# Kernel optimization log

Hardware: AMD Instinct MI355X
Metric: run time of the kernel (lower is better)

The kernel has to match this reference:

```python
import jax, jax.numpy as jnp
import numpy as np

N = 65536      # tokens
H = 8          # num_heads
D = 64         # head_dim
G = 64         # num_slices
HID = H * D    # 512
EPS = 1e-5
SCALE = float(1.0 / np.sqrt(D))


def _lin(k, out_dim, in_dim):
    return (jax.random.normal(k, (out_dim, in_dim), jnp.float32) / np.sqrt(in_dim)).astype(jnp.float32)


def setup_inputs() -> dict:
    key = jax.random.key(0)
    ks = jax.random.split(key, 12)
    return {
        "x": jax.random.normal(ks[0], (N, HID), jnp.float32),
        "W_x": _lin(ks[1], HID, HID), "b_x": jnp.zeros((HID,), jnp.float32),
        "W_slice": _lin(ks[2], G, D), "b_slice": jnp.zeros((G,), jnp.float32),
        "W_t1": _lin(ks[3], G, D), "b_t1": jnp.zeros((G,), jnp.float32),
        "W_t2": _lin(ks[4], 1, G), "b_t2": jnp.zeros((1,), jnp.float32),
        "t_bias": jnp.ones((H, 1, 1), jnp.float32) * 0.5,
        "Wq": _lin(ks[5], D, D), "Wk": _lin(ks[6], D, D),
        "Wv": _lin(ks[7], D, D), "Wo": _lin(ks[8], D, D),
        "W_out": _lin(ks[9], HID, HID), "b_out": jnp.zeros((HID,), jnp.float32),
    }


def reference(x, W_x, b_x, W_slice, b_slice, W_t1, b_t1, W_t2, b_t2,
              t_bias, Wq, Wk, Wv, Wo, W_out, b_out):
    # project and split heads: [N,HID] -> [H,N,D]
    xp = x @ W_x.T + b_x
    x_mid = jnp.transpose(xp.reshape(-1, H, D), (1, 0, 2))

    # per-token temperature MLP: Linear(D,G) -> gelu -> Linear(G,1) -> gelu, + bias
    t = jax.nn.gelu(jax.nn.gelu(x_mid @ W_t1.T + b_t1) @ W_t2.T + b_t2) + t_bias
    t = jnp.clip(t, 0.01)  # [H,N,1]

    # slice logits + gumbel softmax routing weights [H,N,G]
    logits = x_mid @ W_slice.T + b_slice
    u = jax.random.uniform(jax.random.key(1), logits.shape, jnp.float32)
    gnoise = -jnp.log(-jnp.log(u + 1e-8) + 1e-8)
    w = jax.nn.softmax((logits + gnoise) / t, axis=-1)

    # weighted pooling into G slice tokens per head: [H,G,D]
    norm = w.sum(axis=1)  # [H,G]
    tokens = jnp.einsum('hnd,hng->hgd', x_mid, w) / (norm[..., None] + EPS)

    # tiny single-head self-attention over G slice tokens (shared weights, vmapped over H)
    q = tokens @ Wq.T
    k = tokens @ Wk.T
    v = tokens @ Wv.T
    attn = jax.nn.softmax(jnp.einsum('hgd,hGd->hgG', q * SCALE, k), axis=-1)
    o = jnp.einsum('hgG,hGd->hgd', attn, v) @ Wo.T  # [H,G,D]

    # weighted scatter-back to tokens, merge heads, output projection
    out = jnp.einsum('hgd,hng->hnd', o, w)
    out = jnp.transpose(out, (1, 0, 2)).reshape(-1, HID)
    return out @ W_out.T + b_out
```

## Files before the change

### kernel.cpp

```cpp
#include <hip/hip_runtime.h>
#include <stdint.h>

typedef unsigned short u16;
typedef __bf16 bf16x8 __attribute__((ext_vector_type(8)));
typedef float f32x4 __attribute__((ext_vector_type(4)));


__device__ __forceinline__ u16 f2bf(float f) {
  uint32_t u = __float_as_uint(f);
  uint32_t r = u + 0x7fffu + ((u >> 16) & 1u);
  return (u16)(r >> 16);
}
__device__ __forceinline__ float bf2f(u16 h) {
  return __uint_as_float(((uint32_t)h) << 16);
}

union BF8 { bf16x8 v; u16 u[8]; uint4 q4; };

__device__ __forceinline__ float gelu_fast(float x) {
  const float c = 0.79788456080286535588f;
  float z = c * fmaf(0.044715f, x * x * x, x);
  return x / (1.0f + __expf(-2.0f * z));
}

__device__ __forceinline__ uint32_t rotl32(uint32_t v, int s) {
  return (v << s) | (v >> (32 - s));
}

__device__ __forceinline__ uint32_t threefry_bits(uint32_t idx) {
  const uint32_t k0 = 0u, k1 = 1u;
  const uint32_t k2 = 0x1BD11BDAu ^ k0 ^ k1;
  uint32_t x0 = 0u + k0;
  uint32_t x1 = idx + k1;
#define TF_R(r) { x0 += x1; x1 = rotl32(x1, r); x1 ^= x0; }
  TF_R(13) TF_R(15) TF_R(26) TF_R(6)
  x0 += k1; x1 += k2 + 1u;
  TF_R(17) TF_R(29) TF_R(16) TF_R(24)
  x0 += k2; x1 += k0 + 2u;
  TF_R(13) TF_R(15) TF_R(26) TF_R(6)
  x0 += k0; x1 += k1 + 3u;
  TF_R(17) TF_R(29) TF_R(16) TF_R(24)
  x0 += k1; x1 += k2 + 4u;
  TF_R(13) TF_R(15) TF_R(26) TF_R(6)
  x0 += k2; x1 += k0 + 5u;
#undef TF_R
  return x0 ^ x1;
}

__device__ __forceinline__ void gload_lds16(const void* g, void* l) {
  __builtin_amdgcn_global_load_lds(
      (const __attribute__((address_space(1))) void*)g,
      (__attribute__((address_space(3))) void*)l, 16, 0, 0);
}

__global__ __launch_bounds__(256) void conv_split(
    const float* __restrict__ in, u16* __restrict__ hi, u16* __restrict__ lo,
    int nq)
{
  for (int i = blockIdx.x * 256 + threadIdx.x; i < nq; i += gridDim.x * 256) {
    float4 v = ((const float4*)in)[i];
    ushort4 h, l;
    h.x = f2bf(v.x); l.x = f2bf(v.x - bf2f(h.x));
    h.y = f2bf(v.y); l.y = f2bf(v.y - bf2f(h.y));
    h.z = f2bf(v.z); l.z = f2bf(v.z - bf2f(h.z));
    h.w = f2bf(v.w); l.w = f2bf(v.w - bf2f(h.w));
    ((ushort4*)hi)[i] = h;
    ((ushort4*)lo)[i] = l;
  }
}

__global__ __launch_bounds__(256) void gemm_split(
    const u16* __restrict__ Ah, const u16* __restrict__ Al,
    const u16* __restrict__ Bh, const u16* __restrict__ Bl,
    const float* __restrict__ bias, float* __restrict__ C)
{
  __shared__ u16 lds[4][4096];
  const int tid = threadIdx.x;
  const int lane = tid & 63;
  const int w = tid >> 6;
  const int vid = (blockIdx.x & 7) * 256 + (blockIdx.x >> 3);
  const int bn = vid & 3;
  const int bm = vid >> 2;
  const int wr = w >> 1, wc = w & 1;

  f32x4 acc[4][4];
#pragma unroll
  for (int m = 0; m < 4; ++m)
#pragma unroll
    for (int n = 0; n < 4; ++n) acc[m][n] = (f32x4){0.f, 0.f, 0.f, 0.f};

  const int srow = lane >> 2;
  const int scol = (lane & 3) * 8;

  for (int kt = 0; kt < 16; ++kt) {
    const int k0 = kt * 32;
    __syncthreads();
#pragma unroll
    for (int i = 0; i < 8; ++i) {
      const int mat = i & 3;
      const int rb = w * 2 + (i >> 2);
      const int row = rb * 16 + srow;
      const u16* base = (mat == 0) ? Ah : (mat == 1) ? Al
                       : (mat == 2) ? Bh : Bl;
      const int tbase = (mat < 2) ? bm * 128 : bn * 128;
      const u16* src = base + (size_t)(tbase + row) * 512 + k0 + scol;
      gload_lds16(src, &lds[mat][rb * 512]);
    }
    __syncthreads();

    bf16x8 ah[4], al[4], bh_[4], bl_[4];
    const int co = (lane >> 4) * 8;
    const int rr = lane & 15;
#pragma unroll
    for (int f = 0; f < 4; ++f) {
      const int ra  = (wr * 64 + f * 16 + rr) * 32 + co;
      const int rb2 = (wc * 64 + f * 16 + rr) * 32 + co;
      ah[f]  = *(const bf16x8*)&lds[0][ra];
      al[f]  = *(const bf16x8*)&lds[1][ra];
      bh_[f] = *(const bf16x8*)&lds[2][rb2];
      bl_[f] = *(const bf16x8*)&lds[3][rb2];
    }
#pragma unroll
    for (int m = 0; m < 4; ++m)
#pragma unroll
      for (int n = 0; n < 4; ++n) {
        acc[m][n] = __builtin_amdgcn_mfma_f32_16x16x32_bf16(ah[m], bh_[n], acc[m][n], 0, 0, 0);
        acc[m][n] = __builtin_amdgcn_mfma_f32_16x16x32_bf16(ah[m], bl_[n], acc[m][n], 0, 0, 0);
        acc[m][n] = __builtin_amdgcn_mfma_f32_16x16x32_bf16(al[m], bh_[n], acc[m][n], 0, 0, 0);
      }
  }

  const int cn0 = lane & 15;
  const int rm0 = (lane >> 4) * 4;
#pragma unroll
  for (int n = 0; n < 4; ++n) {
    const int ng = bn * 128 + wc * 64 + n * 16 + cn0;
    const float bv = bias[ng];
#pragma unroll
    for (int m = 0; m < 4; ++m) {
      const int mg = bm * 128 + wr * 64 + m * 16 + rm0;
#pragma unroll
      for (int r = 0; r < 4; ++r)
        C[(size_t)(mg + r) * 512 + ng] = acc[m][n][r] + bv;
    }
  }
}

__global__ __launch_bounds__(256) void gemm_packA(
    const uint32_t* __restrict__ A, const u16* __restrict__ Bh,
    const u16* __restrict__ Bl, const float* __restrict__ bias,
    float* __restrict__ C)
{
  __shared__ uint32_t ldsA[128 * 32];
  __shared__ u16 ldsBh[128 * 32], ldsBl[128 * 32];
  const int tid = threadIdx.x;
  const int lane = tid & 63;
  const int w = tid >> 6;
  const int vid = (blockIdx.x & 7) * 256 + (blockIdx.x >> 3);
  const int bn = vid & 3;
  const int bm = vid >> 2;
  const int wr = w >> 1, wcq = w & 1;

  f32x4 acc[4][4];
#pragma unroll
  for (int m = 0; m < 4; ++m)
#pragma unroll
    for (int n = 0; n < 4; ++n) acc[m][n] = (f32x4){0.f, 0.f, 0.f, 0.f};

  for (int kt = 0; kt < 16; ++kt) {
    const int k0 = kt * 32;
    __syncthreads();
#pragma unroll
    for (int i = 0; i < 4; ++i) {
      const int rb8 = i * 4 + w;
      const int row = rb8 * 8 + (lane >> 3);
      const uint32_t* src =
          A + (size_t)(bm * 128 + row) * 512 + k0 + (lane & 7) * 4;
      gload_lds16(src, &ldsA[rb8 * 8 * 32]);
    }
#pragma unroll
    for (int i = 0; i < 2; ++i) {
      const int rb16 = i * 4 + w;
      const int row = rb16 * 16 + (lane >> 2);
      const int sc = (lane & 3) * 8;
      gload_lds16(Bh + (size_t)(bn * 128 + row) * 512 + k0 + sc,
                  &ldsBh[rb16 * 16 * 32]);
      gload_lds16(Bl + (size_t)(bn * 128 + row) * 512 + k0 + sc,
                  &ldsBl[rb16 * 16 * 32]);
    }
    __syncthreads();

    bf16x8 ah[4], al[4], bh_[4], bl_[4];
    const int co = (lane >> 4) * 8;
    const int rr = lane & 15;
#pragma unroll
    for (int f = 0; f < 4; ++f) {
      const int ra = (wr * 64 + f * 16 + rr) * 32 + co;
      const uint4 p0 = *(const uint4*)&ldsA[ra];
      const uint4 p1 = *(const uint4*)&ldsA[ra + 4];
      BF8 hv, lv;
      uint32_t* hd = (uint32_t*)&hv.q4;
      uint32_t* ld = (uint32_t*)&lv.q4;
      hd[0] = __builtin_amdgcn_perm(p0.y, p0.x, 0x05040100u);
      hd[1] = __builtin_amdgcn_perm(p0.w, p0.z, 0x05040100u);
      hd[2] = __builtin_amdgcn_perm(p1.y, p1.x, 0x05040100u);
      hd[3] = __builtin_amdgcn_perm(p1.w, p1.z, 0x05040100u);
      ld[0] = __builtin_amdgcn_perm(p0.y, p0.x, 0x07060302u);
      ld[1] = __builtin_amdgcn_perm(p0.w, p0.z, 0x07060302u);
      ld[2] = __builtin_amdgcn_perm(p1.y, p1.x, 0x07060302u);
      ld[3] = __builtin_amdgcn_perm(p1.w, p1.z, 0x07060302u);
      ah[f] = hv.v; al[f] = lv.v;
      const int rb2 = (wcq * 64 + f * 16 + rr) * 32 + co;
      bh_[f] = *(const bf16x8*)&ldsBh[rb2];
      bl_[f] = *(const bf16x8*)&ldsBl[rb2];
    }
#pragma unroll
    for (int m = 0; m < 4; ++m)
#pragma unroll
      for (int n = 0; n < 4; ++n) {
        acc[m][n] = __builtin_amdgcn_mfma_f32_16x16x32_bf16(ah[m], bh_[n], acc[m][n], 0, 0, 0);
        acc[m][n] = __builtin_amdgcn_mfma_f32_16x16x32_bf16(ah[m], bl_[n], acc[m][n], 0, 0, 0);
        acc[m][n] = __builtin_amdgcn_mfma_f32_16x16x32_bf16(al[m], bh_[n], acc[m][n], 0, 0, 0);
      }
  }

  const int cn0 = lane & 15;
  const int rm0 = (lane >> 4) * 4;
#pragma unroll
  for (int n = 0; n < 4; ++n) {
    const int ng = bn * 128 + wcq * 64 + n * 16 + cn0;
    const float bv = bias[ng];
#pragma unroll
    for (int m = 0; m < 4; ++m) {
      const int mg = bm * 128 + wr * 64 + m * 16 + rm0;
#pragma unroll
      for (int r = 0; r < 4; ++r)
        C[(size_t)(mg + r) * 512 + ng] = acc[m][n][r] + bv;
    }
  }
}

__global__ __launch_bounds__(256, 4) void k2_route(
    const float* __restrict__ xp, const float* __restrict__ Wsl,
    const float* __restrict__ bsl, const float* __restrict__ Wt1,
    const float* __restrict__ bt1, const float* __restrict__ Wt2,
    const float* __restrict__ bt2, const float* __restrict__ tbias,
    uint32_t* __restrict__ wcp)
{
  __shared__ u16 Wf[2][8][2][64][8];
  __shared__ uint32_t wbuf[4][16][68];

  const int tid = threadIdx.x;
  const int l = tid & 63, wid = tid >> 6;
  const int l15 = l & 15, q = l >> 4;
  const int h = blockIdx.x >> 8;
  const int chunk = blockIdx.x & 255;

#pragma unroll
  for (int it = 0; it < 8; ++it) {
    const int slot = tid + it * 256;
    const int p = slot >> 10;
    const int rest = slot & 1023;
    const int nn = rest >> 7;
    const int kk = (rest >> 6) & 1;
    const int sl = rest & 63;
    const int row = nn * 16 + (sl & 15);
    const int kb = kk * 32 + (sl >> 4) * 8;
    const float* src = (row < 64) ? (Wsl + row * 64 + kb)
                                  : (Wt1 + (row - 64) * 64 + kb);
#pragma unroll
    for (int e = 0; e < 8; ++e) {
      const float v = src[e];
      const u16 hb = f2bf(v);
      Wf[p][nn][kk][sl][e] = (p == 0) ? hb : f2bf(v - bf2f(hb));
    }
  }
  __syncthreads();

  float bslv[4], bt1v[4], wt2v[4];
#pragma unroll
  for (int j = 0; j < 4; ++j) {
    bslv[j] = bsl[j * 16 + l15];
    bt1v[j] = bt1[j * 16 + l15];
    wt2v[j] = Wt2[j * 16 + l15];
  }
  const float bt2v = bt2[0], tbv = tbias[h];

#pragma unroll 1
  for (int tm = 0; tm < 4; ++tm) {
    const int n0t = chunk * 256 + (tm >> 1) * 128 + wid * 32 + (tm & 1) * 16;

    bf16x8 ah[2], al[2];
#pragma unroll
    for (int kk = 0; kk < 2; ++kk) {
      const float* sp = xp + (size_t)(n0t + l15) * 512 + h * 64
                        + kk * 32 + q * 8;
      float4 v0 = *(const float4*)sp;
      float4 v1 = *(const float4*)(sp + 4);
      float vv[8] = {v0.x, v0.y, v0.z, v0.w, v1.x, v1.y, v1.z, v1.w};
      BF8 hv, lv;
#pragma unroll
      for (int e = 0; e < 8; ++e) {
        const u16 hb = f2bf(vv[e]);
        hv.u[e] = hb;
        lv.u[e] = f2bf(vv[e] - bf2f(hb));
      }
      ah[kk] = hv.v; al[kk] = lv.v;
    }

    f32x4 acc[8];
#pragma unroll
    for (int n = 0; n < 8; ++n) acc[n] = (f32x4){0.f, 0.f, 0.f, 0.f};
#pragma unroll
    for (int kk = 0; kk < 2; ++kk)
#pragma unroll
      for (int nn = 0; nn < 8; ++nn) {
        BF8 whf, wlf;
        whf.q4 = *(const uint4*)&Wf[0][nn][kk][l][0];
        wlf.q4 = *(const uint4*)&Wf[1][nn][kk][l][0];
        acc[nn] = __builtin_amdgcn_mfma_f32_16x16x32_bf16(ah[kk], whf.v, acc[nn], 0, 0, 0);
        acc[nn] = __builtin_amdgcn_mfma_f32_16x16x32_bf16(ah[kk], wlf.v, acc[nn], 0, 0, 0);
        acc[nn] = __builtin_amdgcn_mfma_f32_16x16x32_bf16(al[kk], whf.v, acc[nn], 0, 0, 0);
      }

    float itv[4];
#pragma unroll
    for (int r = 0; r < 4; ++r) {
      float part = 0.f;
#pragma unroll
      for (int j = 0; j < 4; ++j)
        part += gelu_fast(acc[4 + j][r] + bt1v[j]) * wt2v[j];
      part += __shfl_xor(part, 1);
      part += __shfl_xor(part, 2);
      part += __shfl_xor(part, 4);
      part += __shfl_xor(part, 8);
      const float tval = gelu_fast(part + bt2v) + tbv;
      itv[r] = 1.0f / fmaxf(tval, 0.01f);
    }

    const uint32_t pbase = ((uint32_t)((h << 16) | (n0t + q * 4))) << 6;
#pragma unroll
    for (int j = 0; j < 4; ++j) {
      const uint32_t cc = j * 16 + l15;
#pragma unroll
      for (int r = 0; r < 4; ++r) {
        const uint32_t bits = threefry_bits(pbase + ((uint32_t)r << 6) + cc);
        const float u = __uint_as_float((bits >> 9) | 0x3f800000u) - 1.0f;
        const float gin = -__logf(u + 1e-8f);
        const float gn = -__logf(gin + 1e-8f);
        acc[j][r] = (acc[j][r] + bslv[j] + gn) * itv[r];
      }
    }

#pragma unroll
    for (int r = 0; r < 4; ++r) {
      float mx = fmaxf(fmaxf(acc[0][r], acc[1][r]),
                       fmaxf(acc[2][r], acc[3][r]));
      mx = fmaxf(mx, __shfl_xor(mx, 1));
      mx = fmaxf(mx, __shfl_xor(mx, 2));
      mx = fmaxf(mx, __shfl_xor(mx, 4));
      mx = fmaxf(mx, __shfl_xor(mx, 8));
      float se = 0.f;
#pragma unroll
      for (int j = 0; j < 4; ++j) {
        const float e = __expf(acc[j][r] - mx);
        acc[j][r] = e;
        se += e;
      }
      se += __shfl_xor(se, 1);
      se += __shfl_xor(se, 2);
      se += __shfl_xor(se, 4);
      se += __shfl_xor(se, 8);
      const float inv = 1.0f / se;
#pragma unroll
      for (int j = 0; j < 4; ++j) acc[j][r] *= inv;
    }

#pragma unroll
    for (int j = 0; j < 4; ++j)
#pragma unroll
      for (int r = 0; r < 4; ++r) {
        const float wv = acc[j][r];
        const u16 hb = f2bf(wv);
        const u16 lb = f2bf(wv - bf2f(hb));
        wbuf[wid][q * 4 + r][j * 16 + l15] = (uint32_t)hb | ((uint32_t)lb << 16);
      }
    __syncthreads();

#pragma unroll
    for (int it = 0; it < 4; ++it) {
      const int t = l >> 2;
      const int qq = (l & 3) + it * 4;
      const uint4 v = *(const uint4*)&wbuf[wid][t][qq * 4];
      *(uint4*)(wcp + (size_t)(n0t + t) * 512 + h * 64 + qq * 4) = v;
    }
    __syncthreads();
  }
}

__global__ __launch_bounds__(256) void k3_pool(
    const float* __restrict__ xp, const uint32_t* __restrict__ wcp,
    float* __restrict__ tok_num, float* __restrict__ nrm)
{
  __shared__ float red[64][65];
  __shared__ float redn[64];
  const int h = blockIdx.x >> 7;
  const int chunk = blockIdx.x & 127;
  const int lane = threadIdx.x & 63;
  const int wid = threadIdx.x >> 6;
  const int i0 = (lane & 7) * 8;
  const int j0 = (lane >> 3) * 8;
  const int jq = lane >> 3;

  float acc[8][8];
#pragma unroll
  for (int j = 0; j < 8; ++j)
#pragma unroll
    for (int i = 0; i < 8; ++i) acc[j][i] = 0.f;
  float csum[8];
#pragma unroll
  for (int j = 0; j < 8; ++j) csum[j] = 0.f;

  const int n0 = chunk * 512 + wid * 128;
  const size_t base0 = (size_t)n0 * 512 + h * 64;

  float4 nx0 = *(const float4*)(xp + base0 + i0);
  float4 nx1 = *(const float4*)(xp + base0 + i0 + 4);
  uint4 nq0 = *(const uint4*)(wcp + base0 + j0);
  uint4 nq1 = *(const uint4*)(wcp + base0 + j0 + 4);

#pragma unroll 2
  for (int t = 0; t < 128; ++t) {
    const float4 x0 = nx0, x1 = nx1;
    const uint4 q0 = nq0, q1 = nq1;
    if (t < 127) {
      const size_t nb = base0 + (size_t)(t + 1) * 512;
      nx0 = *(const float4*)(xp + nb + i0);
      nx1 = *(const float4*)(xp + nb + i0 + 4);
      nq0 = *(const uint4*)(wcp + nb + j0);
      nq1 = *(const uint4*)(wcp + nb + j0 + 4);
    }
    const float x8[8] = {x0.x, x0.y, x0.z, x0.w, x1.x, x1.y, x1.z, x1.w};
    const float w8[8] = {
        __uint_as_float(q0.x << 16) + __uint_as_float(q0.x & 0xffff0000u),
        __uint_as_float(q0.y << 16) + __uint_as_float(q0.y & 0xffff0000u),
        __uint_as_float(q0.z << 16) + __uint_as_float(q0.z & 0xffff0000u),
        __uint_as_float(q0.w << 16) + __uint_as_float(q0.w & 0xffff0000u),
        __uint_as_float(q1.x << 16) + __uint_as_float(q1.x & 0xffff0000u),
        __uint_as_float(q1.y << 16) + __uint_as_float(q1.y & 0xffff0000u),
        __uint_as_float(q1.z << 16) + __uint_as_float(q1.z & 0xffff0000u),
        __uint_as_float(q1.w << 16) + __uint_as_float(q1.w & 0xffff0000u)};
#pragma unroll
    for (int j = 0; j < 8; ++j) csum[j] += w8[j];
#pragma unroll
    for (int j = 0; j < 8; ++j)
#pragma unroll
      for (int i = 0; i < 8; ++i)
        acc[j][i] = fmaf(w8[j], x8[i], acc[j][i]);
  }

  for (int w = 0; w < 4; ++w) {
    if (wid == w) {
      if (w == 0) {
#pragma unroll
        for (int j = 0; j < 8; ++j)
#pragma unroll
          for (int i = 0; i < 8; ++i)
            red[j0 + j][i0 | (i ^ jq)] = acc[j][i];
        if ((lane & 7) == 0) {
#pragma unroll
          for (int j = 0; j < 8; ++j) redn[j0 + j] = csum[j];
        }
      } else {
#pragma unroll
        for (int j = 0; j < 8; ++j)
#pragma unroll
          for (int i = 0; i < 8; ++i)
            red[j0 + j][i0 | (i ^ jq)] += acc[j][i];
        if ((lane & 7) == 0) {
#pragma unroll
          for (int j = 0; j < 8; ++j) redn[j0 + j] += csum[j];
        }
      }
    }
    __syncthreads();
  }

  for (int e = threadIdx.x; e < 4096; e += 256) {
    const int g = e >> 6, d = e & 63;
    const int col = (d & 56) | ((d & 7) ^ (g >> 3));
    atomicAdd(&tok_num[h * 4096 + e], red[g][col]);
  }
  if (threadIdx.x < 64)
    atomicAdd(&nrm[h * 64 + threadIdx.x], redn[threadIdx.x]);
}

__global__ __launch_bounds__(256) void k4_attn(
    const float* __restrict__ tok_num, const float* __restrict__ nrm,
    const float* __restrict__ Wq, const float* __restrict__ Wk,
    const float* __restrict__ Wv, const float* __restrict__ Wo,
    float* __restrict__ o_out)
{
  __shared__ float T[64][65], Abuf[64][65], Bbuf[64][65], Wbuf[64][65], S2[64][65];
  const int h = blockIdx.x;
  const int tid = threadIdx.x;

  for (int e = tid; e < 4096; e += 256) {
    const int g = e >> 6, d = e & 63;
    T[g][d] = tok_num[h * 4096 + e] / (nrm[h * 64 + g] + 1e-5f);
  }
  for (int e = tid; e < 4096; e += 256) Wbuf[e >> 6][e & 63] = Wq[e];
  __syncthreads();

  const int g = tid >> 2, d0 = (tid & 3) * 16;
  float r[16];

#pragma unroll
  for (int j = 0; j < 16; ++j) r[j] = 0.f;
  for (int e = 0; e < 64; ++e) {
    const float tv = T[g][e];
#pragma unroll
    for (int j = 0; j < 16; ++j) r[j] = fmaf(tv, Wbuf[d0 + j][e], r[j]);
  }
#pragma unroll
  for (int j = 0; j < 16; ++j) Abuf[g][d0 + j] = r[j];
  __syncthreads();

  for (int e = tid; e < 4096; e += 256) Wbuf[e >> 6][e & 63] = Wk[e];
  __syncthreads();

#pragma unroll
  for (int j = 0; j < 16; ++j) r[j] = 0.f;
  for (int e = 0; e < 64; ++e) {
    const float tv = T[g][e];
#pragma unroll
    for (int j = 0; j < 16; ++j) r[j] = fmaf(tv, Wbuf[d0 + j][e], r[j]);
  }
#pragma unroll
  for (int j = 0; j < 16; ++j) Bbuf[g][d0 + j] = r[j];
  __syncthreads();

#pragma unroll
  for (int j = 0; j < 16; ++j) r[j] = 0.f;
  for (int e = 0; e < 64; ++e) {
    const float qv = Abuf[g][e] * 0.125f;
#pragma unroll
    for (int j = 0; j < 16; ++j) r[j] = fmaf(qv, Bbuf[d0 + j][e], r[j]);
  }
#pragma unroll
  for (int j = 0; j < 16; ++j) S2[g][d0 + j] = r[j];
  __syncthreads();

  if (tid < 64) {
    float mx = -1e30f;
    for (int j = 0; j < 64; ++j) mx = fmaxf(mx, S2[tid][j]);
    float sum = 0.f;
    for (int j = 0; j < 64; ++j) {
      const float e2 = expf(S2[tid][j] - mx);
      S2[tid][j] = e2;
      sum += e2;
    }
    const float inv = 1.0f / sum;
    for (int j = 0; j < 64; ++j) S2[tid][j] *= inv;
  }
  __syncthreads();

  for (int e = tid; e < 4096; e += 256) Wbuf[e >> 6][e & 63] = Wv[e];
  __syncthreads();

#pragma unroll
  for (int j = 0; j < 16; ++j) r[j] = 0.f;
  for (int e = 0; e < 64; ++e) {
    const float tv = T[g][e];
#pragma unroll
    for (int j = 0; j < 16; ++j) r[j] = fmaf(tv, Wbuf[d0 + j][e], r[j]);
  }
  __syncthreads();
#pragma unroll
  for (int j = 0; j < 16; ++j) Bbuf[g][d0 + j] = r[j];
  __syncthreads();

#pragma unroll
  for (int j = 0; j < 16; ++j) r[j] = 0.f;
  for (int e = 0; e < 64; ++e) {
    const float sv = S2[g][e];
#pragma unroll
    for (int j = 0; j < 16; ++j) r[j] = fmaf(sv, Bbuf[e][d0 + j], r[j]);
  }
  __syncthreads();
#pragma unroll
  for (int j = 0; j < 16; ++j) Abuf[g][d0 + j] = r[j];
  for (int e = tid; e < 4096; e += 256) Wbuf[e >> 6][e & 63] = Wo[e];
  __syncthreads();

#pragma unroll
  for (int j = 0; j < 16; ++j) r[j] = 0.f;
  for (int e = 0; e < 64; ++e) {
    const float ov = Abuf[g][e];
#pragma unroll
    for (int j = 0; j < 16; ++j) r[j] = fmaf(ov, Wbuf[d0 + j][e], r[j]);
  }
#pragma unroll
  for (int j = 0; j < 16; ++j) o_out[h * 4096 + g * 64 + d0 + j] = r[j];
}

__global__ __launch_bounds__(256) void k4b_m2(
    const float* __restrict__ o, const float* __restrict__ Wout,
    u16* __restrict__ M2h, u16* __restrict__ M2l)
{
  const int j = blockIdx.x >> 1;
  const int hg = ((blockIdx.x & 1) << 8) + threadIdx.x;
  const int h = hg >> 6;
  const float* orow = &o[hg * 64];
  const float* wrow = &Wout[j * 512 + h * 64];
  float s = 0.f;
#pragma unroll
  for (int d = 0; d < 64; ++d) s = fmaf(orow[d], wrow[d], s);
  const u16 hb = f2bf(s);
  M2h[j * 512 + hg] = hb;
  M2l[j * 512 + hg] = f2bf(s - bf2f(hb));
}

extern "C" void kernel_launch(void* const* d_in, const int* in_sizes, int n_in,
                              void* d_out, int out_size, void* d_ws, size_t ws_size,
                              hipStream_t stream)
{
  const float* x      = (const float*)d_in[0];
  const float* W_x    = (const float*)d_in[1];
  const float* b_x    = (const float*)d_in[2];
  const float* W_sl   = (const float*)d_in[3];
  const float* b_sl   = (const float*)d_in[4];
  const float* W_t1   = (const float*)d_in[5];
  const float* b_t1   = (const float*)d_in[6];
  const float* W_t2   = (const float*)d_in[7];
  const float* b_t2   = (const float*)d_in[8];
  const float* t_bias = (const float*)d_in[9];
  const float* Wq     = (const float*)d_in[10];
  const float* Wk     = (const float*)d_in[11];
  const float* Wv     = (const float*)d_in[12];
  const float* Wo     = (const float*)d_in[13];
  const float* W_out  = (const float*)d_in[14];
  const float* b_out  = (const float*)d_in[15];

  float* out = (float*)d_out;
  float* xp = out;

  char* ws = (char*)d_ws;
  u16*      Ahi   = (u16*)(ws);
  u16*      Alo   = (u16*)(ws + 67108864);
  uint32_t* wcp   = (uint32_t*)(ws);
  u16*      Bhi   = (u16*)(ws + 134217728);
  u16*      Blo   = (u16*)(ws + 134742016);
  float* tok_num  = (float*)(ws + 135266304);
  float* nrm      = (float*)(ws + 135397376);
  float* o_buf    = (float*)(ws + 135399424);

  conv_split<<<2048, 256, 0, stream>>>(x, Ahi, Alo, 8388608);
  conv_split<<<256, 256, 0, stream>>>(W_x, Bhi, Blo, 65536);
  gemm_split<<<2048, 256, 0, stream>>>(Ahi, Alo, Bhi, Blo, b_x, xp);

  hipMemsetAsync(tok_num, 0, 133120, stream);

  k2_route<<<2048, 256, 0, stream>>>(xp, W_sl, b_sl, W_t1, b_t1, W_t2, b_t2,
                                     t_bias, wcp);
  k3_pool<<<1024, 256, 0, stream>>>(xp, wcp, tok_num, nrm);
  k4_attn<<<8, 256, 0, stream>>>(tok_num, nrm, Wq, Wk, Wv, Wo, o_buf);
  k4b_m2<<<1024, 256, 0, stream>>>(o_buf, W_out, Bhi, Blo);
  gemm_packA<<<2048, 256, 0, stream>>>(wcp, Bhi, Blo, b_out, out);
}
```

Measured before the change: 602.0 us.

## Store projected activations as packed bf16 hi/lo and pool with MFMA

The first GEMM now writes its output as packed bf16 hi/lo pairs instead of fp32. The routing kernel then builds its MFMA operands with byte permutes rather than re-splitting floats. The pooling kernel is rewritten from scalar FMA outer products into split-bf16 MFMA accumulation, with half the blocks each covering more tokens. This removes repeated conversion work and moves the pooling arithmetic onto matrix cores, at the cost of three MFMAs per product and a different accumulation order.

```diff
diff --git a/kernel.cpp b/kernel.cpp
--- a/kernel.cpp
+++ b/kernel.cpp
@@ -72,7 +72,7 @@
 __global__ __launch_bounds__(256) void gemm_split(
     const u16* __restrict__ Ah, const u16* __restrict__ Al,
     const u16* __restrict__ Bh, const u16* __restrict__ Bl,
-    const float* __restrict__ bias, float* __restrict__ C)
+    const float* __restrict__ bias, uint32_t* __restrict__ Cp)
 {
   __shared__ u16 lds[4][4096];
   const int tid = threadIdx.x;
@@ -140,8 +140,12 @@
     for (int m = 0; m < 4; ++m) {
       const int mg = bm * 128 + wr * 64 + m * 16 + rm0;
 #pragma unroll
-      for (int r = 0; r < 4; ++r)
-        C[(size_t)(mg + r) * 512 + ng] = acc[m][n][r] + bv;
+      for (int r = 0; r < 4; ++r) {
+        const float v = acc[m][n][r] + bv;
+        const u16 hb = f2bf(v);
+        const u16 lb = f2bf(v - bf2f(hb));
+        Cp[(size_t)(mg + r) * 512 + ng] = (uint32_t)hb | ((uint32_t)lb << 16);
+      }
     }
   }
 }
@@ -241,7 +245,7 @@
 }
 
 __global__ __launch_bounds__(256, 4) void k2_route(
-    const float* __restrict__ xp, const float* __restrict__ Wsl,
+    const uint32_t* __restrict__ xpq, const float* __restrict__ Wsl,
     const float* __restrict__ bsl, const float* __restrict__ Wt1,
     const float* __restrict__ bt1, const float* __restrict__ Wt2,
     const float* __restrict__ bt2, const float* __restrict__ tbias,
@@ -293,18 +297,21 @@
     bf16x8 ah[2], al[2];
 #pragma unroll
     for (int kk = 0; kk < 2; ++kk) {
-      const float* sp = xp + (size_t)(n0t + l15) * 512 + h * 64
-                        + kk * 32 + q * 8;
-      float4 v0 = *(const float4*)sp;
-      float4 v1 = *(const float4*)(sp + 4);
-      float vv[8] = {v0.x, v0.y, v0.z, v0.w, v1.x, v1.y, v1.z, v1.w};
+      const uint32_t* sp = xpq + (size_t)(n0t + l15) * 512 + h * 64
+                           + kk * 32 + q * 8;
+      const uint4 p0 = *(const uint4*)sp;
+      const uint4 p1 = *(const uint4*)(sp + 4);
       BF8 hv, lv;
-#pragma unroll
-      for (int e = 0; e < 8; ++e) {
-        const u16 hb = f2bf(vv[e]);
-        hv.u[e] = hb;
-        lv.u[e] = f2bf(vv[e] - bf2f(hb));
-      }
+      uint32_t* hd = (uint32_t*)&hv.q4;
+      uint32_t* ld = (uint32_t*)&lv.q4;
+      hd[0] = __builtin_amdgcn_perm(p0.y, p0.x, 0x05040100u);
+      hd[1] = __builtin_amdgcn_perm(p0.w, p0.z, 0x05040100u);
+      hd[2] = __builtin_amdgcn_perm(p1.y, p1.x, 0x05040100u);
+      hd[3] = __builtin_amdgcn_perm(p1.w, p1.z, 0x05040100u);
+      ld[0] = __builtin_amdgcn_perm(p0.y, p0.x, 0x07060302u);
+      ld[1] = __builtin_amdgcn_perm(p0.w, p0.z, 0x07060302u);
+      ld[2] = __builtin_amdgcn_perm(p1.y, p1.x, 0x07060302u);
+      ld[3] = __builtin_amdgcn_perm(p1.w, p1.z, 0x07060302u);
       ah[kk] = hv.v; al[kk] = lv.v;
     }
 
@@ -398,101 +405,98 @@
   }
 }
 
-__global__ __launch_bounds__(256) void k3_pool(
-    const float* __restrict__ xp, const uint32_t* __restrict__ wcp,
+__global__ __launch_bounds__(256, 2) void k3_pool(
+    const uint32_t* __restrict__ xpq, const uint32_t* __restrict__ wcp,
     float* __restrict__ tok_num, float* __restrict__ nrm)
 {
   __shared__ float red[64][65];
-  __shared__ float redn[64];
-  const int h = blockIdx.x >> 7;
-  const int chunk = blockIdx.x & 127;
+  const int h = blockIdx.x >> 6;
+  const int chunk = blockIdx.x & 63;
   const int lane = threadIdx.x & 63;
   const int wid = threadIdx.x >> 6;
-  const int i0 = (lane & 7) * 8;
-  const int j0 = (lane >> 3) * 8;
-  const int jq = lane >> 3;
-
-  float acc[8][8];
-#pragma unroll
-  for (int j = 0; j < 8; ++j)
-#pragma unroll
-    for (int i = 0; i < 8; ++i) acc[j][i] = 0.f;
-  float csum[8];
-#pragma unroll
-  for (int j = 0; j < 8; ++j) csum[j] = 0.f;
-
-  const int n0 = chunk * 512 + wid * 128;
-  const size_t base0 = (size_t)n0 * 512 + h * 64;
-
-  float4 nx0 = *(const float4*)(xp + base0 + i0);
-  float4 nx1 = *(const float4*)(xp + base0 + i0 + 4);
-  uint4 nq0 = *(const uint4*)(wcp + base0 + j0);
-  uint4 nq1 = *(const uint4*)(wcp + base0 + j0 + 4);
-
-#pragma unroll 2
-  for (int t = 0; t < 128; ++t) {
-    const float4 x0 = nx0, x1 = nx1;
-    const uint4 q0 = nq0, q1 = nq1;
-    if (t < 127) {
-      const size_t nb = base0 + (size_t)(t + 1) * 512;
-      nx0 = *(const float4*)(xp + nb + i0);
-      nx1 = *(const float4*)(xp + nb + i0 + 4);
-      nq0 = *(const uint4*)(wcp + nb + j0);
-      nq1 = *(const uint4*)(wcp + nb + j0 + 4);
-    }
-    const float x8[8] = {x0.x, x0.y, x0.z, x0.w, x1.x, x1.y, x1.z, x1.w};
-    const float w8[8] = {
-        __uint_as_float(q0.x << 16) + __uint_as_float(q0.x & 0xffff0000u),
-        __uint_as_float(q0.y << 16) + __uint_as_float(q0.y & 0xffff0000u),
-        __uint_as_float(q0.z << 16) + __uint_as_float(q0.z & 0xffff0000u),
-        __uint_as_float(q0.w << 16) + __uint_as_float(q0.w & 0xffff0000u),
-        __uint_as_float(q1.x << 16) + __uint_as_float(q1.x & 0xffff0000u),
-        __uint_as_float(q1.y << 16) + __uint_as_float(q1.y & 0xffff0000u),
-        __uint_as_float(q1.z << 16) + __uint_as_float(q1.z & 0xffff0000u),
-        __uint_as_float(q1.w << 16) + __uint_as_float(q1.w & 0xffff0000u)};
-#pragma unroll
-    for (int j = 0; j < 8; ++j) csum[j] += w8[j];
-#pragma unroll
-    for (int j = 0; j < 8; ++j)
-#pragma unroll
-      for (int i = 0; i < 8; ++i)
-        acc[j][i] = fmaf(w8[j], x8[i], acc[j][i]);
+  const int l15 = lane & 15, q = lane >> 4;
+
+  f32x4 acc[4][4];
+#pragma unroll
+  for (int m = 0; m < 4; ++m)
+#pragma unroll
+    for (int n = 0; n < 4; ++n) acc[m][n] = (f32x4){0.f, 0.f, 0.f, 0.f};
+  float csum[4] = {0.f, 0.f, 0.f, 0.f};
+
+  const int tw = chunk * 1024 + wid * 256;
+#pragma unroll 1
+  for (int tt = 0; tt < 8; ++tt) {
+    const int t0 = tw + tt * 32;
+    uint32_t wreg[4][8], xreg[4][8];
+#pragma unroll
+    for (int e = 0; e < 8; ++e) {
+      const size_t rb = (size_t)(t0 + q * 8 + e) * 512 + h * 64 + l15;
+#pragma unroll
+      for (int m = 0; m < 4; ++m) {
+        wreg[m][e] = wcp[rb + m * 16];
+        xreg[m][e] = xpq[rb + m * 16];
+      }
+    }
+    bf16x8 whf[4], wlf[4], xhf[4], xlf[4];
+#pragma unroll
+    for (int m = 0; m < 4; ++m) {
+      BF8 hv, lv, xh, xl;
+      uint32_t* hd = (uint32_t*)&hv.q4;
+      uint32_t* ld = (uint32_t*)&lv.q4;
+      uint32_t* xhd = (uint32_t*)&xh.q4;
+      uint32_t* xld = (uint32_t*)&xl.q4;
+#pragma unroll
+      for (int p = 0; p < 4; ++p) {
+        hd[p]  = __builtin_amdgcn_perm(wreg[m][2*p+1], wreg[m][2*p], 0x05040100u);
+        ld[p]  = __builtin_amdgcn_perm(wreg[m][2*p+1], wreg[m][2*p], 0x07060302u);
+        xhd[p] = __builtin_amdgcn_perm(xreg[m][2*p+1], xreg[m][2*p], 0x05040100u);
+        xld[p] = __builtin_amdgcn_perm(xreg[m][2*p+1], xreg[m][2*p], 0x07060302u);
+      }
+      whf[m] = hv.v; wlf[m] = lv.v; xhf[m] = xh.v; xlf[m] = xl.v;
+#pragma unroll
+      for (int e = 0; e < 8; ++e)
+        csum[m] += __uint_as_float(wreg[m][e] << 16)
+                 + __uint_as_float(wreg[m][e] & 0xffff0000u);
+    }
+#pragma unroll
+    for (int m = 0; m < 4; ++m)
+#pragma unroll
+      for (int n = 0; n < 4; ++n) {
+        acc[m][n] = __builtin_amdgcn_mfma_f32_16x16x32_bf16(whf[m], xhf[n], acc[m][n], 0, 0, 0);
+        acc[m][n] = __builtin_amdgcn_mfma_f32_16x16x32_bf16(whf[m], xlf[n], acc[m][n], 0, 0, 0);
+        acc[m][n] = __builtin_amdgcn_mfma_f32_16x16x32_bf16(wlf[m], xhf[n], acc[m][n], 0, 0, 0);
+      }
+  }
+
+#pragma unroll
+  for (int m = 0; m < 4; ++m) {
+    csum[m] += __shfl_xor(csum[m], 16);
+    csum[m] += __shfl_xor(csum[m], 32);
+  }
+  if (q == 0) {
+#pragma unroll
+    for (int m = 0; m < 4; ++m)
+      atomicAdd(&nrm[h * 64 + m * 16 + l15], csum[m]);
   }
 
   for (int w = 0; w < 4; ++w) {
     if (wid == w) {
-      if (w == 0) {
-#pragma unroll
-        for (int j = 0; j < 8; ++j)
-#pragma unroll
-          for (int i = 0; i < 8; ++i)
-            red[j0 + j][i0 | (i ^ jq)] = acc[j][i];
-        if ((lane & 7) == 0) {
-#pragma unroll
-          for (int j = 0; j < 8; ++j) redn[j0 + j] = csum[j];
-        }
-      } else {
-#pragma unroll
-        for (int j = 0; j < 8; ++j)
-#pragma unroll
-          for (int i = 0; i < 8; ++i)
-            red[j0 + j][i0 | (i ^ jq)] += acc[j][i];
-        if ((lane & 7) == 0) {
-#pragma unroll
-          for (int j = 0; j < 8; ++j) redn[j0 + j] += csum[j];
-        }
-      }
+#pragma unroll
+      for (int m = 0; m < 4; ++m)
+#pragma unroll
+        for (int n = 0; n < 4; ++n)
+#pragma unroll
+          for (int r = 0; r < 4; ++r) {
+            const int g = m * 16 + q * 4 + r;
+            const int d = n * 16 + l15;
+            if (w == 0) red[g][d] = acc[m][n][r];
+            else        red[g][d] += acc[m][n][r];
+          }
     }
     __syncthreads();
   }
-
-  for (int e = threadIdx.x; e < 4096; e += 256) {
-    const int g = e >> 6, d = e & 63;
-    const int col = (d & 56) | ((d & 7) ^ (g >> 3));
-    atomicAdd(&tok_num[h * 4096 + e], red[g][col]);
-  }
-  if (threadIdx.x < 64)
-    atomicAdd(&nrm[h * 64 + threadIdx.x], redn[threadIdx.x]);
+  for (int e = threadIdx.x; e < 4096; e += 256)
+    atomicAdd(&tok_num[h * 4096 + e], red[e >> 6][e & 63]);
 }
 
 __global__ __launch_bounds__(256) void k4_attn(
@@ -643,7 +647,7 @@
   const float* b_out  = (const float*)d_in[15];
 
   float* out = (float*)d_out;
-  float* xp = out;
+  uint32_t* xpq = (uint32_t*)d_out;
 
   char* ws = (char*)d_ws;
   u16*      Ahi   = (u16*)(ws);
@@ -657,13 +661,13 @@
 
   conv_split<<<2048, 256, 0, stream>>>(x, Ahi, Alo, 8388608);
   conv_split<<<256, 256, 0, stream>>>(W_x, Bhi, Blo, 65536);
-  gemm_split<<<2048, 256, 0, stream>>>(Ahi, Alo, Bhi, Blo, b_x, xp);
+  gemm_split<<<2048, 256, 0, stream>>>(Ahi, Alo, Bhi, Blo, b_x, xpq);
 
   hipMemsetAsync(tok_num, 0, 133120, stream);
 
-  k2_route<<<2048, 256, 0, stream>>>(xp, W_sl, b_sl, W_t1, b_t1, W_t2, b_t2,
+  k2_route<<<2048, 256, 0, stream>>>(xpq, W_sl, b_sl, W_t1, b_t1, W_t2, b_t2,
                                      t_bias, wcp);
-  k3_pool<<<1024, 256, 0, stream>>>(xp, wcp, tok_num, nrm);
+  k3_pool<<<512, 256, 0, stream>>>(xpq, wcp, tok_num, nrm);
   k4_attn<<<8, 256, 0, stream>>>(tok_num, nrm, Wq, Wk, Wv, Wo, o_buf);
   k4b_m2<<<1024, 256, 0, stream>>>(o_buf, W_out, Bhi, Blo);
   gemm_packA<<<2048, 256, 0, stream>>>(wcp, Bhi, Blo, b_out, out);
```

Measured after the change: 554.9 us, median of 2. 1.08x faster.
